# Performance work log

Hardware: AMD Instinct MI355X
Metric: run time of the kernel (lower is better)

Reference implementation:

```python
import jax, jax.numpy as jnp
import numpy as np

EMBED = 2048
NUM_EXPERTS = 64
TOP_K = 8


def setup_inputs() -> dict:
    key = jax.random.key(0)
    k1, k2, k3 = jax.random.split(key, 3)
    inputs = jax.random.normal(k1, (8, 4096, EMBED), dtype=jnp.float32)
    # nn.Linear(embed_size, num_experts): weight [num_experts, embed_size], bias [num_experts]
    W = jax.random.normal(k2, (NUM_EXPERTS, EMBED), dtype=jnp.float32) / np.sqrt(EMBED)
    b = jax.random.normal(k3, (NUM_EXPERTS,), dtype=jnp.float32) * 0.01
    return {"inputs": inputs, "W": W, "b": b}


def reference(inputs, W, b):
    # Linear projection: [B, S, E] x [E, N] -> [B, S, N]
    logits = jnp.einsum('bse,ne->bsn', inputs, W) + b
    # top-k selection along expert axis
    _, indices = jax.lax.top_k(logits, TOP_K)  # [B, S, K] int32
    # scatter mask: 1 at selected experts (one_hot sum == scatter_ of ones)
    mask = jax.nn.one_hot(indices, NUM_EXPERTS, dtype=jnp.bool_).any(axis=-2)  # [B, S, N]
    # masked_fill(-inf) + softmax -> probs only on selected experts
    masked = jnp.where(mask, logits, -jnp.inf)
    probs = jax.nn.softmax(masked, axis=-1)
    return probs, indices
```

## Files before the change

kernel.cpp:

```cpp
#include <hip/hip_runtime.h>
#include <cmath>

#define NTOK 32768
#define EMB  2048
#define NEXP 64
#define TOPK 8
#define BT   64
#define KC   32
#define NCH  (EMB / KC)
#define TAU  1e-4f

typedef __attribute__((ext_vector_type(8))) short bf16x8;
typedef __attribute__((ext_vector_type(4))) float f32x4;

union U4 { unsigned int u[4]; bf16x8 v; };

__device__ __forceinline__ float uf(unsigned int x) { return __uint_as_float(x); }
__device__ __forceinline__ unsigned int fu(float x) { return __float_as_uint(x); }

__device__ __forceinline__ void gld16(const float* g, float* lds) {
    __builtin_amdgcn_global_load_lds(
        (const __attribute__((address_space(1))) void*)g,
        (__attribute__((address_space(3))) void*)lds,
        16, 0, 0);
}

__global__ __launch_bounds__(512, 2) void router_bf16x3(
    const float* __restrict__ X,
    const float* __restrict__ W,
    const float* __restrict__ Bv,
    float* __restrict__ out)
{
    __shared__ __align__(16) unsigned char smem[40960];
    float* xsBase          = (float*)smem;
    unsigned short* wsBase = (unsigned short*)(smem + 16384);
    float* lg              = (float*)smem;

    const int tid  = threadIdx.x;
    const int lane = tid & 63;
    const int w    = tid >> 6;
    const int tg   = w >> 1;
    const int eh   = w & 1;
    const int eL   = lane & 15;
    const int q    = lane >> 4;
    const int t0   = blockIdx.x * BT;

    f32x4 am[2], ac[2];
    #pragma unroll
    for (int t = 0; t < 2; ++t) {
        am[t] = (f32x4){0.f, 0.f, 0.f, 0.f};
        ac[t] = (f32x4){0.f, 0.f, 0.f, 0.f};
    }

    auto stageX = [&](int ch, int buf) {
        const int kc0 = ch * KC;
        float* dst = xsBase + buf * 2048;
        const int row = w * 8 + (lane >> 3);
        const int g   = (lane & 7) ^ (lane >> 3);
        gld16(&X[(size_t)(t0 + row) * EMB + kc0 + 4 * g], dst + w * 256);
    };

    auto loadW = [&](int ch) -> float4 {
        const int er = tid >> 3;
        const int h  = tid & 7;
        return *(const float4*)&W[(size_t)er * EMB + ch * KC + 4 * h];
    };
    auto putW = [&](float4 v, int buf) {
        const int er = tid >> 3, h = tid & 7, slot = h >> 1, sub = h & 1;
        unsigned short* base = wsBase + buf * 6144;
        unsigned int u0 = fu(v.x), u1 = fu(v.y), u2 = fu(v.z), u3 = fu(v.w);
        unsigned int p1a = (u0 >> 16) | (u1 & 0xffff0000u);
        unsigned int p1b = (u2 >> 16) | (u3 & 0xffff0000u);
        float r0 = v.x - uf(u0 & 0xffff0000u), r1 = v.y - uf(u1 & 0xffff0000u);
        float r2 = v.z - uf(u2 & 0xffff0000u), r3 = v.w - uf(u3 & 0xffff0000u);
        unsigned int w0 = fu(r0), w1 = fu(r1), w2 = fu(r2), w3 = fu(r3);
        unsigned int p2a = (w0 >> 16) | (w1 & 0xffff0000u);
        unsigned int p2b = (w2 >> 16) | (w3 & 0xffff0000u);
        float s0 = r0 - uf(w0 & 0xffff0000u), s1 = r1 - uf(w1 & 0xffff0000u);
        float s2 = r2 - uf(w2 & 0xffff0000u), s3 = r3 - uf(w3 & 0xffff0000u);
        unsigned int p3a = (fu(s0) >> 16) | (fu(s1) & 0xffff0000u);
        unsigned int p3b = (fu(s2) >> 16) | (fu(s3) & 0xffff0000u);
        const int off = slot * 512 + er * 8 + sub * 4;
        *(uint2*)(void*)(base + off)          = make_uint2(p1a, p1b);
        *(uint2*)(void*)(base + 2048 + off)   = make_uint2(p2a, p2b);
        *(uint2*)(void*)(base + 4096 + off)   = make_uint2(p3a, p3b);
    };

    auto compute = [&](int buf) {
        const float* xb          = xsBase + buf * 2048;
        const unsigned short* wb = wsBase + buf * 6144;
        bf16x8 Bf[2][3];
        #pragma unroll
        for (int cc = 0; cc < 2; ++cc) {
            const int er = eh * 32 + cc * 16 + eL;
            #pragma unroll
            for (int p = 0; p < 3; ++p)
                Bf[cc][p] = *(const bf16x8*)(const void*)(wb + p * 2048 + q * 512 + er * 8);
        }
        const int row = tg * 16 + eL;
        const int sl  = (2 * q) ^ (eL & 7);
        const float4 aL = *(const float4*)&xb[row * 32 + 4 * sl];
        const float4 aH = *(const float4*)&xb[row * 32 + 4 * (sl ^ 1)];
        U4 A1, A2, A3;
        const float e0[8] = {aL.x, aL.y, aL.z, aL.w, aH.x, aH.y, aH.z, aH.w};
        #pragma unroll
        for (int m = 0; m < 4; ++m) {
            float x0 = e0[2*m], x1 = e0[2*m+1];
            unsigned int u0 = fu(x0), u1 = fu(x1);
            A1.u[m] = (u0 >> 16) | (u1 & 0xffff0000u);
            float r0 = x0 - uf(u0 & 0xffff0000u), r1 = x1 - uf(u1 & 0xffff0000u);
            unsigned int w0 = fu(r0), w1 = fu(r1);
            A2.u[m] = (w0 >> 16) | (w1 & 0xffff0000u);
            float s0 = r0 - uf(w0 & 0xffff0000u), s1 = r1 - uf(w1 & 0xffff0000u);
            A3.u[m] = (fu(s0) >> 16) | (fu(s1) & 0xffff0000u);
        }
        #pragma unroll
        for (int cc = 0; cc < 2; ++cc) {
            am[cc] = __builtin_amdgcn_mfma_f32_16x16x32_bf16(A1.v, Bf[cc][0], am[cc], 0,0,0);
            ac[cc] = __builtin_amdgcn_mfma_f32_16x16x32_bf16(A1.v, Bf[cc][1], ac[cc], 0,0,0);
            ac[cc] = __builtin_amdgcn_mfma_f32_16x16x32_bf16(A2.v, Bf[cc][0], ac[cc], 0,0,0);
            ac[cc] = __builtin_amdgcn_mfma_f32_16x16x32_bf16(A1.v, Bf[cc][2], ac[cc], 0,0,0);
            ac[cc] = __builtin_amdgcn_mfma_f32_16x16x32_bf16(A2.v, Bf[cc][1], ac[cc], 0,0,0);
            ac[cc] = __builtin_amdgcn_mfma_f32_16x16x32_bf16(A3.v, Bf[cc][0], ac[cc], 0,0,0);
        }
    };

    stageX(0, 0);
    putW(loadW(0), 0);
    __syncthreads();
    for (int ch = 0; ch < NCH; ++ch) {
        const int cur = ch & 1;
        const bool pf = (ch + 1 < NCH);
        float4 nw;
        if (pf) { stageX(ch + 1, cur ^ 1); nw = loadW(ch + 1); }
        compute(cur);
        if (pf) putW(nw, cur ^ 1);
        __syncthreads();
    }

    float* probs = out;
    float* idxo  = out + (size_t)NTOK * NEXP;
    const float bb0 = Bv[eh * 32 + eL];
    const float bb1 = Bv[eh * 32 + 16 + eL];
    #pragma unroll
    for (int cc = 0; cc < 2; ++cc) {
        const int e = eh * 32 + cc * 16 + eL;
        const float bbv = cc ? bb1 : bb0;
        #pragma unroll
        for (int i = 0; i < 4; ++i) {
            const int r = tg * 16 + q * 4 + i;
            lg[r * 66 + e] = (am[cc][i] + ac[cc][i]) + bbv;
        }
    }
    __syncthreads();

    auto slowToken = [&](int Tg) {
        const float* xr = X + (size_t)Tg * EMB;
        const float* wr = W + (size_t)lane * EMB;
        double s0 = 0.0, s1 = 0.0, s2 = 0.0, s3 = 0.0;
        for (int k = 0; k < EMB; k += 16) {
            const float4 xa = *(const float4*)&xr[k];
            const float4 xb = *(const float4*)&xr[k + 4];
            const float4 xc = *(const float4*)&xr[k + 8];
            const float4 xd = *(const float4*)&xr[k + 12];
            const float4 wa = *(const float4*)&wr[k];
            const float4 wb = *(const float4*)&wr[k + 4];
            const float4 wc = *(const float4*)&wr[k + 8];
            const float4 wd = *(const float4*)&wr[k + 12];
            s0 += (double)xa.x * wa.x + (double)xa.y * wa.y
                + (double)xa.z * wa.z + (double)xa.w * wa.w;
            s1 += (double)xb.x * wb.x + (double)xb.y * wb.y
                + (double)xb.z * wb.z + (double)xb.w * wb.w;
            s2 += (double)xc.x * wc.x + (double)xc.y * wc.y
                + (double)xc.z * wc.z + (double)xc.w * wc.w;
            s3 += (double)xd.x * wd.x + (double)xd.y * wd.y
                + (double)xd.z * wd.z + (double)xd.w * wd.w;
        }
        double ex = (double)Bv[lane] + ((s0 + s1) + (s2 + s3));
        bool selb = false; int myrank = 0;
        double m0d = 0.0; float ss = 0.f;
        #pragma unroll
        for (int it = 0; it < TOPK; ++it) {
            double bv = selb ? -1.0e300 : ex; int be = lane;
            #pragma unroll
            for (int off = 1; off <= 32; off <<= 1) {
                const double ov = __shfl_xor(bv, off, 64);
                const int    oe = __shfl_xor(be, off, 64);
                if (ov > bv || (ov == bv && oe < be)) { bv = ov; be = oe; }
            }
            if (it == 0) m0d = bv;
            ss += __expf((float)(bv - m0d));
            if (lane == be) { selb = true; myrank = it; }
        }
        probs[(size_t)Tg * NEXP + lane] = selb ? __expf((float)(ex - m0d)) / ss : 0.f;
        if (selb) idxo[(size_t)Tg * TOPK + myrank] = (float)lane;
    };

    #pragma unroll
    for (int i = 0; i < 2; ++i) {
        const int T = w * 8 + i * 4 + q;
        float v[4];
        #pragma unroll
        for (int c = 0; c < 4; ++c) v[c] = lg[T * 66 + c * 16 + eL];

        unsigned sel = 0;
        float m0 = 0.f, ssum = 0.f, prev = 0.f, mingap = 1e30f;
        int myIdx = 0;
        #pragma unroll
        for (int it = 0; it <= TOPK; ++it) {
            float bv = -1e30f; int be = 1 << 30;
            #pragma unroll
            for (int c = 0; c < 4; ++c)
                if (!((sel >> c) & 1) && v[c] > bv) { bv = v[c]; be = c * 16 + eL; }
            float gv = bv; int ge = be;
            #pragma unroll
            for (int off = 1; off <= 8; off <<= 1) {
                const float ov = __shfl_xor(gv, off, 64);
                const int   oe = __shfl_xor(ge, off, 64);
                if (ov > gv || (ov == gv && oe < ge)) { gv = ov; ge = oe; }
            }
            if (it == 0) m0 = gv;
            else mingap = fminf(mingap, prev - gv);
            prev = gv;
            if (it < TOPK) {
                ssum += __expf(gv - m0);
                if ((ge & 15) == eL) sel |= 1u << (ge >> 4);
                if (eL == it) myIdx = ge;
            }
        }
        const int Tg = t0 + T;
        const float inv = 1.0f / ssum;
        #pragma unroll
        for (int c = 0; c < 4; ++c) {
            const float p = ((sel >> c) & 1) ? __expf(v[c] - m0) * inv : 0.0f;
            probs[(size_t)Tg * NEXP + c * 16 + eL] = p;
        }
        if (eL < TOPK) idxo[(size_t)Tg * TOPK + eL] = (float)myIdx;

        const unsigned long long fb = __ballot(mingap < TAU);
        for (int q2 = 0; q2 < 4; ++q2)
            if ((fb >> (q2 * 16)) & 1) slowToken(t0 + w * 8 + i * 4 + q2);
    }
}

extern "C" void kernel_launch(void* const* d_in, const int* in_sizes, int n_in,
                              void* d_out, int out_size, void* d_ws, size_t ws_size,
                              hipStream_t stream) {
    const float* X = (const float*)d_in[0];
    const float* W = (const float*)d_in[1];
    const float* B = (const float*)d_in[2];
    router_bf16x3<<<NTOK / BT, 512, 0, stream>>>(X, W, B, (float*)d_out);
}
```

Measured before the change: 484.9 us.

## Presplit W into bf16x3 in a prepass and stream via direct LDS loads

A separate kernel now converts W into three bf16 pieces once per launch and stores them in a global buffer in the LDS layout. The main kernel then stages both X and the presplit W into LDS with global_load_lds, which removes per-block W conversion and register round-trips. The K chunk doubles to 64, so there are half as many barriers, and the pipeline uses explicit vmcnt waits with raw s_barrier. In exchange LDS use doubles to 80KB, which may reduce occupancy below 2 blocks per CU, and there is an extra kernel launch.

```diff
diff --git a/kernel.cpp b/kernel.cpp
--- a/kernel.cpp
+++ b/kernel.cpp
@@ -6,7 +6,7 @@
 #define NEXP 64
 #define TOPK 8
 #define BT   64
-#define KC   32
+#define KC   64
 #define NCH  (EMB / KC)
 #define TAU  1e-4f
 
@@ -15,25 +15,55 @@
 
 union U4 { unsigned int u[4]; bf16x8 v; };
 
-__device__ __forceinline__ float uf(unsigned int x) { return __uint_as_float(x); }
-__device__ __forceinline__ unsigned int fu(float x) { return __float_as_uint(x); }
-
-__device__ __forceinline__ void gld16(const float* g, float* lds) {
+__device__ unsigned short g_wl[NCH][12288];
+
+static __device__ __forceinline__ float uf(unsigned int x) { return __uint_as_float(x); }
+static __device__ __forceinline__ unsigned int fu(float x) { return __float_as_uint(x); }
+
+__device__ __forceinline__ void gld16(const void* g, void* lds) {
     __builtin_amdgcn_global_load_lds(
         (const __attribute__((address_space(1))) void*)g,
         (__attribute__((address_space(3))) void*)lds,
         16, 0, 0);
 }
 
-__global__ __launch_bounds__(512, 2) void router_bf16x3(
+__global__ __launch_bounds__(512) void wsplit(const float* __restrict__ W) {
+    const int ch  = blockIdx.x;
+    const int tid = threadIdx.x;
+    const int er = tid >> 3, kk = (tid >> 2) & 1, q = tid & 3;
+    const int k0 = ch * KC + kk * 32 + q * 8;
+    const float* src = &W[(size_t)er * EMB + k0];
+    float x[8];
+    #pragma unroll
+    for (int j = 0; j < 8; ++j) x[j] = src[j];
+    unsigned int P[3][4];
+    #pragma unroll
+    for (int m = 0; m < 4; ++m) {
+        float x0 = x[2*m], x1 = x[2*m+1];
+        unsigned int u0 = fu(x0), u1 = fu(x1);
+        P[0][m] = (u0 >> 16) | (u1 & 0xffff0000u);
+        float r0 = x0 - uf(u0 & 0xffff0000u), r1 = x1 - uf(u1 & 0xffff0000u);
+        unsigned int w0 = fu(r0), w1 = fu(r1);
+        P[1][m] = (w0 >> 16) | (w1 & 0xffff0000u);
+        float s0 = r0 - uf(w0 & 0xffff0000u), s1 = r1 - uf(w1 & 0xffff0000u);
+        P[2][m] = (fu(s0) >> 16) | (fu(s1) & 0xffff0000u);
+    }
+    #pragma unroll
+    for (int p = 0; p < 3; ++p) {
+        unsigned short* d = &g_wl[ch][((p*2 + kk)*4 + q)*512 + er*8];
+        *(uint4*)(void*)d = make_uint4(P[p][0], P[p][1], P[p][2], P[p][3]);
+    }
+}
+
+__global__ __launch_bounds__(512, 2) void router_mx(
     const float* __restrict__ X,
     const float* __restrict__ W,
     const float* __restrict__ Bv,
     float* __restrict__ out)
 {
-    __shared__ __align__(16) unsigned char smem[40960];
+    __shared__ __align__(16) unsigned char smem[81920];
     float* xsBase          = (float*)smem;
-    unsigned short* wsBase = (unsigned short*)(smem + 16384);
+    unsigned short* wsBase = (unsigned short*)(smem + 32768);
     float* lg              = (float*)smem;
 
     const int tid  = threadIdx.x;
@@ -52,90 +82,83 @@
         ac[t] = (f32x4){0.f, 0.f, 0.f, 0.f};
     }
 
-    auto stageX = [&](int ch, int buf) {
-        const int kc0 = ch * KC;
-        float* dst = xsBase + buf * 2048;
-        const int row = w * 8 + (lane >> 3);
-        const int g   = (lane & 7) ^ (lane >> 3);
-        gld16(&X[(size_t)(t0 + row) * EMB + kc0 + 4 * g], dst + w * 256);
+    auto stage = [&](int ch, int buf) {
+        float* xd = xsBase + buf * 4096;
+        #pragma unroll
+        for (int j = 0; j < 2; ++j) {
+            const int rb  = (w * 2 + j) * 4;
+            const int row = rb + (lane >> 4);
+            const int gl  = (lane & 15) ^ (row & 7);
+            gld16(&X[(size_t)(t0 + row) * EMB + ch * KC + 4 * gl], xd + rb * 64);
+        }
+        unsigned short* wd = wsBase + buf * 12288;
+        const unsigned short* wsrc = &g_wl[ch][0];
+        #pragma unroll
+        for (int j = 0; j < 3; ++j) {
+            const int o = (w * 3 + j) * 512;
+            gld16(wsrc + o + lane * 8, wd + o);
+        }
     };
 
-    auto loadW = [&](int ch) -> float4 {
-        const int er = tid >> 3;
-        const int h  = tid & 7;
-        return *(const float4*)&W[(size_t)er * EMB + ch * KC + 4 * h];
+    auto compute = [&](int buf) {
+        const float* xb          = xsBase + buf * 4096;
+        const unsigned short* wb = wsBase + buf * 12288;
+        const int row = tg * 16 + eL;
+        #pragma unroll
+        for (int kk = 0; kk < 2; ++kk) {
+            bf16x8 Bf0[3], Bf1[3];
+            #pragma unroll
+            for (int p = 0; p < 3; ++p) {
+                const int seg = ((p * 2 + kk) * 4 + q) * 512;
+                Bf0[p] = *(const bf16x8*)(const void*)(wb + seg + (eh * 32 + eL) * 8);
+                Bf1[p] = *(const bf16x8*)(const void*)(wb + seg + (eh * 32 + 16 + eL) * 8);
+            }
+            const int g0 = kk * 8 + ((2 * q) ^ (row & 7));
+            const int g1 = kk * 8 + ((2 * q + 1) ^ (row & 7));
+            const float4 aL = *(const float4*)&xb[row * 64 + 4 * g0];
+            const float4 aH = *(const float4*)&xb[row * 64 + 4 * g1];
+            U4 A1, A2, A3;
+            const float e0[8] = {aL.x, aL.y, aL.z, aL.w, aH.x, aH.y, aH.z, aH.w};
+            #pragma unroll
+            for (int m = 0; m < 4; ++m) {
+                float x0 = e0[2*m], x1 = e0[2*m+1];
+                unsigned int u0 = fu(x0), u1 = fu(x1);
+                A1.u[m] = (u0 >> 16) | (u1 & 0xffff0000u);
+                float r0 = x0 - uf(u0 & 0xffff0000u), r1 = x1 - uf(u1 & 0xffff0000u);
+                unsigned int w0 = fu(r0), w1 = fu(r1);
+                A2.u[m] = (w0 >> 16) | (w1 & 0xffff0000u);
+                float s0 = r0 - uf(w0 & 0xffff0000u), s1 = r1 - uf(w1 & 0xffff0000u);
+                A3.u[m] = (fu(s0) >> 16) | (fu(s1) & 0xffff0000u);
+            }
+            am[0] = __builtin_amdgcn_mfma_f32_16x16x32_bf16(A1.v, Bf0[0], am[0], 0,0,0);
+            ac[0] = __builtin_amdgcn_mfma_f32_16x16x32_bf16(A1.v, Bf0[1], ac[0], 0,0,0);
+            ac[0] = __builtin_amdgcn_mfma_f32_16x16x32_bf16(A2.v, Bf0[0], ac[0], 0,0,0);
+            ac[0] = __builtin_amdgcn_mfma_f32_16x16x32_bf16(A1.v, Bf0[2], ac[0], 0,0,0);
+            ac[0] = __builtin_amdgcn_mfma_f32_16x16x32_bf16(A2.v, Bf0[1], ac[0], 0,0,0);
+            ac[0] = __builtin_amdgcn_mfma_f32_16x16x32_bf16(A3.v, Bf0[0], ac[0], 0,0,0);
+            am[1] = __builtin_amdgcn_mfma_f32_16x16x32_bf16(A1.v, Bf1[0], am[1], 0,0,0);
+            ac[1] = __builtin_amdgcn_mfma_f32_16x16x32_bf16(A1.v, Bf1[1], ac[1], 0,0,0);
+            ac[1] = __builtin_amdgcn_mfma_f32_16x16x32_bf16(A2.v, Bf1[0], ac[1], 0,0,0);
+            ac[1] = __builtin_amdgcn_mfma_f32_16x16x32_bf16(A1.v, Bf1[2], ac[1], 0,0,0);
+            ac[1] = __builtin_amdgcn_mfma_f32_16x16x32_bf16(A2.v, Bf1[1], ac[1], 0,0,0);
+            ac[1] = __builtin_amdgcn_mfma_f32_16x16x32_bf16(A3.v, Bf1[0], ac[1], 0,0,0);
+        }
     };
-    auto putW = [&](float4 v, int buf) {
-        const int er = tid >> 3, h = tid & 7, slot = h >> 1, sub = h & 1;
-        unsigned short* base = wsBase + buf * 6144;
-        unsigned int u0 = fu(v.x), u1 = fu(v.y), u2 = fu(v.z), u3 = fu(v.w);
-        unsigned int p1a = (u0 >> 16) | (u1 & 0xffff0000u);
-        unsigned int p1b = (u2 >> 16) | (u3 & 0xffff0000u);
-        float r0 = v.x - uf(u0 & 0xffff0000u), r1 = v.y - uf(u1 & 0xffff0000u);
-        float r2 = v.z - uf(u2 & 0xffff0000u), r3 = v.w - uf(u3 & 0xffff0000u);
-        unsigned int w0 = fu(r0), w1 = fu(r1), w2 = fu(r2), w3 = fu(r3);
-        unsigned int p2a = (w0 >> 16) | (w1 & 0xffff0000u);
-        unsigned int p2b = (w2 >> 16) | (w3 & 0xffff0000u);
-        float s0 = r0 - uf(w0 & 0xffff0000u), s1 = r1 - uf(w1 & 0xffff0000u);
-        float s2 = r2 - uf(w2 & 0xffff0000u), s3 = r3 - uf(w3 & 0xffff0000u);
-        unsigned int p3a = (fu(s0) >> 16) | (fu(s1) & 0xffff0000u);
-        unsigned int p3b = (fu(s2) >> 16) | (fu(s3) & 0xffff0000u);
-        const int off = slot * 512 + er * 8 + sub * 4;
-        *(uint2*)(void*)(base + off)          = make_uint2(p1a, p1b);
-        *(uint2*)(void*)(base + 2048 + off)   = make_uint2(p2a, p2b);
-        *(uint2*)(void*)(base + 4096 + off)   = make_uint2(p3a, p3b);
-    };
-
-    auto compute = [&](int buf) {
-        const float* xb          = xsBase + buf * 2048;
-        const unsigned short* wb = wsBase + buf * 6144;
-        bf16x8 Bf[2][3];
-        #pragma unroll
-        for (int cc = 0; cc < 2; ++cc) {
-            const int er = eh * 32 + cc * 16 + eL;
-            #pragma unroll
-            for (int p = 0; p < 3; ++p)
-                Bf[cc][p] = *(const bf16x8*)(const void*)(wb + p * 2048 + q * 512 + er * 8);
-        }
-        const int row = tg * 16 + eL;
-        const int sl  = (2 * q) ^ (eL & 7);
-        const float4 aL = *(const float4*)&xb[row * 32 + 4 * sl];
-        const float4 aH = *(const float4*)&xb[row * 32 + 4 * (sl ^ 1)];
-        U4 A1, A2, A3;
-        const float e0[8] = {aL.x, aL.y, aL.z, aL.w, aH.x, aH.y, aH.z, aH.w};
-        #pragma unroll
-        for (int m = 0; m < 4; ++m) {
-            float x0 = e0[2*m], x1 = e0[2*m+1];
-            unsigned int u0 = fu(x0), u1 = fu(x1);
-            A1.u[m] = (u0 >> 16) | (u1 & 0xffff0000u);
-            float r0 = x0 - uf(u0 & 0xffff0000u), r1 = x1 - uf(u1 & 0xffff0000u);
-            unsigned int w0 = fu(r0), w1 = fu(r1);
-            A2.u[m] = (w0 >> 16) | (w1 & 0xffff0000u);
-            float s0 = r0 - uf(w0 & 0xffff0000u), s1 = r1 - uf(w1 & 0xffff0000u);
-            A3.u[m] = (fu(s0) >> 16) | (fu(s1) & 0xffff0000u);
-        }
-        #pragma unroll
-        for (int cc = 0; cc < 2; ++cc) {
-            am[cc] = __builtin_amdgcn_mfma_f32_16x16x32_bf16(A1.v, Bf[cc][0], am[cc], 0,0,0);
-            ac[cc] = __builtin_amdgcn_mfma_f32_16x16x32_bf16(A1.v, Bf[cc][1], ac[cc], 0,0,0);
-            ac[cc] = __builtin_amdgcn_mfma_f32_16x16x32_bf16(A2.v, Bf[cc][0], ac[cc], 0,0,0);
-            ac[cc] = __builtin_amdgcn_mfma_f32_16x16x32_bf16(A1.v, Bf[cc][2], ac[cc], 0,0,0);
-            ac[cc] = __builtin_amdgcn_mfma_f32_16x16x32_bf16(A2.v, Bf[cc][1], ac[cc], 0,0,0);
-            ac[cc] = __builtin_amdgcn_mfma_f32_16x16x32_bf16(A3.v, Bf[cc][0], ac[cc], 0,0,0);
-        }
-    };
-
-    stageX(0, 0);
-    putW(loadW(0), 0);
-    __syncthreads();
+
+    stage(0, 0);
     for (int ch = 0; ch < NCH; ++ch) {
         const int cur = ch & 1;
-        const bool pf = (ch + 1 < NCH);
-        float4 nw;
-        if (pf) { stageX(ch + 1, cur ^ 1); nw = loadW(ch + 1); }
+        if (ch + 1 < NCH) {
+            stage(ch + 1, cur ^ 1);
+            asm volatile("s_waitcnt vmcnt(5)" ::: "memory");
+        } else {
+            asm volatile("s_waitcnt vmcnt(0)" ::: "memory");
+        }
+        __builtin_amdgcn_s_barrier();
+        asm volatile("" ::: "memory");
         compute(cur);
-        if (pf) putW(nw, cur ^ 1);
-        __syncthreads();
+        asm volatile("" ::: "memory");
+        __builtin_amdgcn_s_barrier();
     }
 
     float* probs = out;
@@ -249,5 +272,6 @@
     const float* X = (const float*)d_in[0];
     const float* W = (const float*)d_in[1];
     const float* B = (const float*)d_in[2];
-    router_bf16x3<<<NTOK / BT, 512, 0, stream>>>(X, W, B, (float*)d_out);
-}
+    wsplit<<<NCH, 512, 0, stream>>>(W);
+    router_mx<<<NTOK / BT, 512, 0, stream>>>(X, W, B, (float*)d_out);
+}
```

After: 510.5 us. +5.3%, slower.
